# Optimization experiments

Hardware: AMD Instinct MI355X
Metric: run time of the kernel (lower is better)

The kernel has to match this reference:

```python
import jax, jax.numpy as jnp
import numpy as np

CHUNK = 64  # output-column tile to bound the [M, K, CHUNK] intermediate


def _mam(A, B):
    """Multiply-and-max/min 'matmul': C[m,n] = max_k(A[m,k]*B[k,n]) + min_k(A[m,k]*B[k,n]).
    A: [M, K], B: [K, N]. Tiled over N to avoid materializing [M, K, N]."""
    M, K = A.shape
    N = B.shape[1]
    assert N % CHUNK == 0
    # [N/CHUNK, K, CHUNK]
    B_tiles = B.reshape(K, N // CHUNK, CHUNK).transpose(1, 0, 2)

    def step(carry, B_blk):
        # prod: [M, K, CHUNK]
        prod = A[:, :, None] * B_blk[None, :, :]
        out = prod.max(axis=1) + prod.min(axis=1)  # [M, CHUNK]
        return carry, out

    _, tiles = jax.lax.scan(step, 0, B_tiles)  # [N/CHUNK, M, CHUNK]
    return tiles.transpose(1, 0, 2).reshape(M, N)


def setup_inputs() -> dict:
    key = jax.random.key(0)
    k1, k2, k3 = jax.random.split(key, 3)
    M, K, N = 2048, 1024, 1024
    x = jax.random.normal(k1, (M, K), dtype=jnp.float32)
    # torch stores weight as [out_features, in_features]
    weight = jax.random.normal(k2, (N, K), dtype=jnp.float32) * (1.0 / np.sqrt(K))
    bias = jax.random.normal(k3, (N,), dtype=jnp.float32) * (1.0 / np.sqrt(K))
    return {"x": x, "weight": weight, "bias": bias}


def reference(x, weight, bias):
    # beta == 0 (beta=False): forward is MAM(x, W^T) + bias
    C = _mam(x, weight.T)
    return C + bias[None, :]
```

## Files before the change

### kernel.cpp

```cpp
#include <hip/hip_runtime.h>
#include <math.h>


#define TS 64
#define BK 16
#define LDSP 68
#define STRIPF (BK * LDSP)

__device__ __forceinline__ void mam_upd(float& mx, float& mn, float p0, float p1) {
    asm("v_max3_f32 %0, %1, %2, %0" : "+v"(mx) : "v"(p0), "v"(p1));
    asm("v_min3_f32 %0, %1, %2, %0" : "+v"(mn) : "v"(p0), "v"(p1));
}

__global__
__attribute__((amdgpu_flat_work_group_size(256, 256)))
__attribute__((amdgpu_waves_per_eu(2, 2)))
void mam_sk(
    const float* __restrict__ A, const float* __restrict__ W,
    const float* __restrict__ bias, float* __restrict__ C,
    int M, int N, int K)
{
    __shared__ __align__(16) float smem[8 * STRIPF];
    float* cmx = smem;
    float* cmn = smem + TS * TS;

    const int t    = threadIdx.x;
    const int w    = t >> 6;
    const int lane = t & 63;
    const int ty   = lane >> 3;
    const int tx   = lane & 7;
    const int m0   = blockIdx.y * TS;
    const int n0   = blockIdx.x * TS;
    const int kc   = K >> 2;
    const int kb0  = w * kc;

    const int sr = lane >> 2;
    const int sc = lane & 3;

    float* sAw = smem + (size_t)w * STRIPF;
    float* sWw = smem + (size_t)(4 + w) * STRIPF;

    const float* Ap = A + (size_t)(m0 + sr) * K + kb0 + sc * 4;
    const float* Wp = W + (size_t)(n0 + sr) * K + kb0 + sc * 4;

    float mx[8][8], mn[8][8];
#pragma unroll
    for (int i = 0; i < 8; ++i)
#pragma unroll
        for (int j = 0; j < 8; ++j) {
            mx[i][j] = -INFINITY;
            mn[i][j] =  INFINITY;
        }

    float4 ra[4], rw[4];
#pragma unroll
    for (int q = 0; q < 4; ++q) {
        ra[q] = *(const float4*)(Ap + (size_t)q * 16 * K);
        rw[q] = *(const float4*)(Wp + (size_t)q * 16 * K);
    }
    Ap += BK;
    Wp += BK;

    const int nStages = kc / BK;
    for (int s = 0; s < nStages; ++s) {
#pragma unroll
        for (int q = 0; q < 4; ++q) {
            const int mI = sr + q * 16;
            sAw[(sc * 4 + 0) * LDSP + mI] = ra[q].x;
            sAw[(sc * 4 + 1) * LDSP + mI] = ra[q].y;
            sAw[(sc * 4 + 2) * LDSP + mI] = ra[q].z;
            sAw[(sc * 4 + 3) * LDSP + mI] = ra[q].w;
            sWw[(sc * 4 + 0) * LDSP + mI] = rw[q].x;
            sWw[(sc * 4 + 1) * LDSP + mI] = rw[q].y;
            sWw[(sc * 4 + 2) * LDSP + mI] = rw[q].z;
            sWw[(sc * 4 + 3) * LDSP + mI] = rw[q].w;
        }
        if (s + 1 < nStages) {
#pragma unroll
            for (int q = 0; q < 4; ++q) {
                ra[q] = *(const float4*)(Ap + (size_t)q * 16 * K);
                rw[q] = *(const float4*)(Wp + (size_t)q * 16 * K);
            }
            Ap += BK;
            Wp += BK;
        }

#pragma unroll
        for (int k = 0; k < BK; k += 2) {
            float4 a00 = *(const float4*)&sAw[(k    ) * LDSP + ty * 8];
            float4 a01 = *(const float4*)&sAw[(k    ) * LDSP + ty * 8 + 4];
            float4 a10 = *(const float4*)&sAw[(k + 1) * LDSP + ty * 8];
            float4 a11 = *(const float4*)&sAw[(k + 1) * LDSP + ty * 8 + 4];
            float4 w00 = *(const float4*)&sWw[(k    ) * LDSP + tx * 8];
            float4 w01 = *(const float4*)&sWw[(k    ) * LDSP + tx * 8 + 4];
            float4 w10 = *(const float4*)&sWw[(k + 1) * LDSP + tx * 8];
            float4 w11 = *(const float4*)&sWw[(k + 1) * LDSP + tx * 8 + 4];

            float a0[8] = {a00.x, a00.y, a00.z, a00.w, a01.x, a01.y, a01.z, a01.w};
            float a1[8] = {a10.x, a10.y, a10.z, a10.w, a11.x, a11.y, a11.z, a11.w};
            float b0[8] = {w00.x, w00.y, w00.z, w00.w, w01.x, w01.y, w01.z, w01.w};
            float b1[8] = {w10.x, w10.y, w10.z, w10.w, w11.x, w11.y, w11.z, w11.w};

#pragma unroll
            for (int i = 0; i < 8; ++i)
#pragma unroll
                for (int j = 0; j < 8; ++j) {
                    float p0 = a0[i] * b0[j];
                    float p1 = a1[i] * b1[j];
                    mam_upd(mx[i][j], mn[i][j], p0, p1);
                }
        }
    }

    __syncthreads();

    for (int rnd = 0; rnd < 4; ++rnd) {
        if (w == rnd) {
#pragma unroll
            for (int i = 0; i < 8; ++i)
#pragma unroll
                for (int j = 0; j < 8; ++j) {
                    const int idx = (ty * 8 + i) * TS + tx * 8 + j;
                    if (rnd == 0) {
                        cmx[idx] = mx[i][j];
                        cmn[idx] = mn[i][j];
                    } else {
                        cmx[idx] = fmaxf(cmx[idx], mx[i][j]);
                        cmn[idx] = fminf(cmn[idx], mn[i][j]);
                    }
                }
        }
        __syncthreads();
    }

    float4 blo = *(const float4*)(bias + n0 + tx * 8);
    float4 bhi = *(const float4*)(bias + n0 + tx * 8 + 4);
#pragma unroll
    for (int i2 = 0; i2 < 2; ++i2) {
        const int i   = w * 2 + i2;
        const int row = ty * 8 + i;
        const int idx = row * TS + tx * 8;
        float4 o0, o1;
        o0.x = cmx[idx + 0] + cmn[idx + 0] + blo.x;
        o0.y = cmx[idx + 1] + cmn[idx + 1] + blo.y;
        o0.z = cmx[idx + 2] + cmn[idx + 2] + blo.z;
        o0.w = cmx[idx + 3] + cmn[idx + 3] + blo.w;
        o1.x = cmx[idx + 4] + cmn[idx + 4] + bhi.x;
        o1.y = cmx[idx + 5] + cmn[idx + 5] + bhi.y;
        o1.z = cmx[idx + 6] + cmn[idx + 6] + bhi.z;
        o1.w = cmx[idx + 7] + cmn[idx + 7] + bhi.w;
        float4* p = (float4*)(C + (size_t)(m0 + row) * N + n0 + tx * 8);
        p[0] = o0;
        p[1] = o1;
    }
}

#define BM 64
#define BN 64
#define FBK 32
#define LDSW 68

__device__ __forceinline__ void mam_upd_fb(float& mx, float& mn, float p0, float p1) {
    float nmx, nmn;
    asm("v_max3_f32 %0, %1, %2, %3" : "=v"(nmx) : "v"(p0), "v"(p1), "v"(mx));
    asm("v_min3_f32 %0, %1, %2, %3" : "=v"(nmn) : "v"(p0), "v"(p1), "v"(mn));
    mx = nmx;
    mn = nmn;
}

__global__ __launch_bounds__(256) void mam_fallback(
    const float* __restrict__ A, const float* __restrict__ W,
    const float* __restrict__ bias, float* __restrict__ C,
    int M, int N, int K)
{
    __shared__ float Asf[FBK][LDSW];
    __shared__ float Wsf[FBK][LDSW];

    const int t  = threadIdx.x;
    const int tx = t & 15;
    const int ty = t >> 4;
    const int m0 = blockIdx.y * BM;
    const int n0 = blockIdx.x * BN;
    const int r  = t >> 3;
    const int kq = t & 7;

    const float* Aptr = A + (size_t)(m0 + r) * K + kq * 4;
    const float* Wptr = W + (size_t)(n0 + r) * K + kq * 4;

    float vmax[4][4], vmin[4][4];
#pragma unroll
    for (int i = 0; i < 4; ++i)
#pragma unroll
        for (int j = 0; j < 4; ++j) {
            vmax[i][j] = -INFINITY;
            vmin[i][j] =  INFINITY;
        }

    for (int k0 = 0; k0 < K; k0 += FBK) {
        float4 a0 = *(const float4*)(Aptr);
        float4 a1 = *(const float4*)(Aptr + (size_t)32 * K);
        float4 w0 = *(const float4*)(Wptr);
        float4 w1 = *(const float4*)(Wptr + (size_t)32 * K);
        Aptr += FBK;
        Wptr += FBK;

        const int kk = kq * 4;
        Asf[kk + 0][r]      = a0.x;
        Asf[kk + 1][r]      = a0.y;
        Asf[kk + 2][r]      = a0.z;
        Asf[kk + 3][r]      = a0.w;
        Asf[kk + 0][r + 32] = a1.x;
        Asf[kk + 1][r + 32] = a1.y;
        Asf[kk + 2][r + 32] = a1.z;
        Asf[kk + 3][r + 32] = a1.w;

        Wsf[kk + 0][r]      = w0.x;
        Wsf[kk + 1][r]      = w0.y;
        Wsf[kk + 2][r]      = w0.z;
        Wsf[kk + 3][r]      = w0.w;
        Wsf[kk + 0][r + 32] = w1.x;
        Wsf[kk + 1][r + 32] = w1.y;
        Wsf[kk + 2][r + 32] = w1.z;
        Wsf[kk + 3][r + 32] = w1.w;

        __syncthreads();

#pragma unroll
        for (int k = 0; k < FBK; k += 2) {
            float4 ta0 = *(const float4*)&Asf[k    ][ty * 4];
            float4 ta1 = *(const float4*)&Asf[k + 1][ty * 4];
            float4 tb0 = *(const float4*)&Wsf[k    ][tx * 4];
            float4 tb1 = *(const float4*)&Wsf[k + 1][tx * 4];

            float a0v[4] = {ta0.x, ta0.y, ta0.z, ta0.w};
            float a1v[4] = {ta1.x, ta1.y, ta1.z, ta1.w};
            float b0v[4] = {tb0.x, tb0.y, tb0.z, tb0.w};
            float b1v[4] = {tb1.x, tb1.y, tb1.z, tb1.w};

#pragma unroll
            for (int i = 0; i < 4; ++i)
#pragma unroll
                for (int j = 0; j < 4; ++j) {
                    float p0 = a0v[i] * b0v[j];
                    float p1 = a1v[i] * b1v[j];
                    mam_upd_fb(vmax[i][j], vmin[i][j], p0, p1);
                }
        }
        __syncthreads();
    }

    float4 bv = *(const float4*)(bias + n0 + tx * 4);
#pragma unroll
    for (int i = 0; i < 4; ++i) {
        float4 o;
        o.x = vmax[i][0] + vmin[i][0] + bv.x;
        o.y = vmax[i][1] + vmin[i][1] + bv.y;
        o.z = vmax[i][2] + vmin[i][2] + bv.z;
        o.w = vmax[i][3] + vmin[i][3] + bv.w;
        *(float4*)(C + (size_t)(m0 + ty * 4 + i) * N + n0 + tx * 4) = o;
    }
}

extern "C" void kernel_launch(void* const* d_in, const int* in_sizes, int n_in,
                              void* d_out, int out_size, void* d_ws, size_t ws_size,
                              hipStream_t stream) {
    const float* x    = (const float*)d_in[0];
    const float* w    = (const float*)d_in[1];
    const float* bias = (const float*)d_in[2];
    float* out = (float*)d_out;

    const int N = in_sizes[2];
    const int K = in_sizes[1] / N;
    const int M = in_sizes[0] / K;

    const bool fast_ok = (K % (4 * BK) == 0) && (M % TS == 0) && (N % TS == 0);

    if (fast_ok) {
        dim3 grid(N / TS, M / TS);
        mam_sk<<<grid, 256, 0, stream>>>(x, w, bias, out, M, N, K);
    } else {
        dim3 grid(N / BN, M / BM);
        mam_fallback<<<grid, 256, 0, stream>>>(x, w, bias, out, M, N, K);
    }
}
```

Before: 156.1 us.

## Interleave k-pairs in LDS and use packed FP32 multiply for products

Rewrites the shared-memory layout so each row stores consecutive k-pairs interleaved per m index (stride 132), letting each thread load adjacent (k, k+1) values as f32x2. The two products per element are then computed with one v_pk_mul_f32 instead of two scalar multiplies, before the max3/min3 update. This aims to cut VALU multiply instructions in the inner loop. In exchange it changes LDS store patterns (float2 stores) and may add bank conflicts or register pressure from packed operands.

```diff
diff --git a/kernel.cpp b/kernel.cpp
--- a/kernel.cpp
+++ b/kernel.cpp
@@ -4,12 +4,20 @@
 
 #define TS 64
 #define BK 16
-#define LDSP 68
-#define STRIPF (BK * LDSP)
-
-__device__ __forceinline__ void mam_upd(float& mx, float& mn, float p0, float p1) {
-    asm("v_max3_f32 %0, %1, %2, %0" : "+v"(mx) : "v"(p0), "v"(p1));
-    asm("v_min3_f32 %0, %1, %2, %0" : "+v"(mn) : "v"(p0), "v"(p1));
+#define RS 132
+#define STRIPF (8 * RS)
+
+typedef __attribute__((ext_vector_type(2))) float f32x2;
+typedef __attribute__((ext_vector_type(4))) float f32x4;
+
+__device__ __forceinline__ f32x2 lo2(f32x4 v) { return __builtin_shufflevector(v, v, 0, 1); }
+__device__ __forceinline__ f32x2 hi2(f32x4 v) { return __builtin_shufflevector(v, v, 2, 3); }
+
+__device__ __forceinline__ void mam_upd_pk(float& mx, float& mn, f32x2 a, f32x2 b) {
+    f32x2 p;
+    asm("v_pk_mul_f32 %0, %1, %2" : "=v"(p) : "v"(a), "v"(b));
+    asm("v_max3_f32 %0, %1, %2, %0" : "+v"(mx) : "v"(p.x), "v"(p.y));
+    asm("v_min3_f32 %0, %1, %2, %0" : "+v"(mn) : "v"(p.x), "v"(p.y));
 }
 
 __global__
@@ -66,14 +74,10 @@
 #pragma unroll
         for (int q = 0; q < 4; ++q) {
             const int mI = sr + q * 16;
-            sAw[(sc * 4 + 0) * LDSP + mI] = ra[q].x;
-            sAw[(sc * 4 + 1) * LDSP + mI] = ra[q].y;
-            sAw[(sc * 4 + 2) * LDSP + mI] = ra[q].z;
-            sAw[(sc * 4 + 3) * LDSP + mI] = ra[q].w;
-            sWw[(sc * 4 + 0) * LDSP + mI] = rw[q].x;
-            sWw[(sc * 4 + 1) * LDSP + mI] = rw[q].y;
-            sWw[(sc * 4 + 2) * LDSP + mI] = rw[q].z;
-            sWw[(sc * 4 + 3) * LDSP + mI] = rw[q].w;
+            *(float2*)&sAw[(sc * 2 + 0) * RS + mI * 2] = make_float2(ra[q].x, ra[q].y);
+            *(float2*)&sAw[(sc * 2 + 1) * RS + mI * 2] = make_float2(ra[q].z, ra[q].w);
+            *(float2*)&sWw[(sc * 2 + 0) * RS + mI * 2] = make_float2(rw[q].x, rw[q].y);
+            *(float2*)&sWw[(sc * 2 + 1) * RS + mI * 2] = make_float2(rw[q].z, rw[q].w);
         }
         if (s + 1 < nStages) {
 #pragma unroll
@@ -86,29 +90,28 @@
         }
 
 #pragma unroll
-        for (int k = 0; k < BK; k += 2) {
-            float4 a00 = *(const float4*)&sAw[(k    ) * LDSP + ty * 8];
-            float4 a01 = *(const float4*)&sAw[(k    ) * LDSP + ty * 8 + 4];
-            float4 a10 = *(const float4*)&sAw[(k + 1) * LDSP + ty * 8];
-            float4 a11 = *(const float4*)&sAw[(k + 1) * LDSP + ty * 8 + 4];
-            float4 w00 = *(const float4*)&sWw[(k    ) * LDSP + tx * 8];
-            float4 w01 = *(const float4*)&sWw[(k    ) * LDSP + tx * 8 + 4];
-            float4 w10 = *(const float4*)&sWw[(k + 1) * LDSP + tx * 8];
-            float4 w11 = *(const float4*)&sWw[(k + 1) * LDSP + tx * 8 + 4];
-
-            float a0[8] = {a00.x, a00.y, a00.z, a00.w, a01.x, a01.y, a01.z, a01.w};
-            float a1[8] = {a10.x, a10.y, a10.z, a10.w, a11.x, a11.y, a11.z, a11.w};
-            float b0[8] = {w00.x, w00.y, w00.z, w00.w, w01.x, w01.y, w01.z, w01.w};
-            float b1[8] = {w10.x, w10.y, w10.z, w10.w, w11.x, w11.y, w11.z, w11.w};
+        for (int kp = 0; kp < BK / 2; ++kp) {
+            const float* rA = sAw + kp * RS + ty * 16;
+            const float* rW = sWw + kp * RS + tx * 16;
+            f32x4 A0 = *(const f32x4*)(rA + 0);
+            f32x4 A1 = *(const f32x4*)(rA + 4);
+            f32x4 A2 = *(const f32x4*)(rA + 8);
+            f32x4 A3 = *(const f32x4*)(rA + 12);
+            f32x4 W0 = *(const f32x4*)(rW + 0);
+            f32x4 W1 = *(const f32x4*)(rW + 4);
+            f32x4 W2 = *(const f32x4*)(rW + 8);
+            f32x4 W3 = *(const f32x4*)(rW + 12);
+
+            f32x2 av[8] = {lo2(A0), hi2(A0), lo2(A1), hi2(A1),
+                           lo2(A2), hi2(A2), lo2(A3), hi2(A3)};
+            f32x2 bv[8] = {lo2(W0), hi2(W0), lo2(W1), hi2(W1),
+                           lo2(W2), hi2(W2), lo2(W3), hi2(W3)};
 
 #pragma unroll
             for (int i = 0; i < 8; ++i)
 #pragma unroll
-                for (int j = 0; j < 8; ++j) {
-                    float p0 = a0[i] * b0[j];
-                    float p1 = a1[i] * b1[j];
-                    mam_upd(mx[i][j], mn[i][j], p0, p1);
-                }
+                for (int j = 0; j < 8; ++j)
+                    mam_upd_pk(mx[i][j], mn[i][j], av[i], bv[j]);
         }
     }
 
```

Result: slower. 170.8 us (+9.4%).
